# Performance work log

Measured on AMD Instinct MI355X. Metric: run time of the kernel, lower is better.

The kernel has to match this reference:

```python
import jax, jax.numpy as jnp
import numpy as np

EMBED = 1024
HEADS = 16
HEAD_DIM = EMBED // HEADS


def setup_inputs() -> dict:
    key = jax.random.key(0)
    ks = jax.random.split(key, 8)
    N, S, E = 4, 2048, EMBED
    inp = {
        "queries": jax.random.normal(ks[0], (N, S, E), dtype=jnp.float32),
        "keys": jax.random.normal(ks[1], (N, S, E), dtype=jnp.float32),
        "values": jax.random.normal(ks[2], (N, S, E), dtype=jnp.float32),
        # projection weights, stored as (in, out) so y = x @ W
        "Wq": jax.random.normal(ks[3], (E, E), dtype=jnp.float32) / np.sqrt(E),
        "Wk": jax.random.normal(ks[4], (E, E), dtype=jnp.float32) / np.sqrt(E),
        "Wv": jax.random.normal(ks[5], (E, E), dtype=jnp.float32) / np.sqrt(E),
        "Wo": jax.random.normal(ks[6], (E, E), dtype=jnp.float32) / np.sqrt(E),
        "bo": jax.random.normal(ks[7], (E,), dtype=jnp.float32) * 0.01,
    }
    return inp


def reference(queries, keys, values, Wq, Wk, Wv, Wo, bo):
    N, Sq, E = queries.shape
    Sk = keys.shape[1]
    H, D = HEADS, HEAD_DIM
    # linear projections (no bias)
    q = (queries @ Wq).reshape(N, Sq, H, D)
    k = (keys @ Wk).reshape(N, Sk, H, D)
    v = (values @ Wv).reshape(N, Sk, H, D)
    # energy: [N, H, Sq, Sk]
    energy = jnp.einsum("nqhd,nkhd->nhqk", q, k)
    attn = jax.nn.softmax(energy / np.sqrt(D).astype(np.float32), axis=3)
    # out: [N, Sq, H, D] -> [N, Sq, E]
    out = jnp.einsum("nhqk,nkhd->nqhd", attn, v).reshape(N, Sq, E)
    return out @ Wo + bo
```

## Files before the change

### kernel.cpp

```cpp
#include <hip/hip_runtime.h>
#include <hip/hip_bf16.h>

typedef __bf16 bf16;
typedef bf16 bf16x4v __attribute__((ext_vector_type(4)));
typedef bf16 bf16x8 __attribute__((ext_vector_type(8)));
typedef float f32x4 __attribute__((ext_vector_type(4)));
typedef float f32x16 __attribute__((ext_vector_type(16)));
typedef unsigned int uint;
typedef unsigned short ushort;

static constexpr int E   = 1024;
static constexpr int SEQ = 2048;
static constexpr int NB  = 4;
static constexpr int M   = NB * SEQ;

__device__ __forceinline__ void async16(const void* g, void* l) {
  __builtin_amdgcn_global_load_lds(
      (const __attribute__((address_space(1))) void*)g,
      (__attribute__((address_space(3))) void*)l, 16, 0, 0);
}

__device__ __forceinline__ uint pack2(float a, float b) {
  bf16 x = (bf16)a, y = (bf16)b;
  return (uint)__builtin_bit_cast(ushort, x) |
         ((uint)__builtin_bit_cast(ushort, y) << 16);
}

__global__ __launch_bounds__(256) void k_conv3(const float* __restrict__ s0,
                                               const float* __restrict__ s1,
                                               const float* __restrict__ s2,
                                               bf16* __restrict__ d0,
                                               bf16* __restrict__ d1,
                                               bf16* __restrict__ d2) {
  const float* src = blockIdx.z == 0 ? s0 : blockIdx.z == 1 ? s1 : s2;
  bf16* dst        = blockIdx.z == 0 ? d0 : blockIdx.z == 1 ? d1 : d2;
  size_t i = (size_t)blockIdx.x * 256 + threadIdx.x;
  const float4* s = reinterpret_cast<const float4*>(src) + i * 2;
  float4 a = s[0], b = s[1];
  bf16x8 o;
  o[0] = (bf16)a.x; o[1] = (bf16)a.y; o[2] = (bf16)a.z; o[3] = (bf16)a.w;
  o[4] = (bf16)b.x; o[5] = (bf16)b.y; o[6] = (bf16)b.z; o[7] = (bf16)b.w;
  *reinterpret_cast<bf16x8*>(dst + i * 8) = o;
}

__global__ __launch_bounds__(256) void k_convW(const float* s0, const float* s1,
                                               const float* s2, const float* s3,
                                               bf16* d0, bf16* d1, bf16* d2, bf16* d3) {
  __shared__ float tile[64][65];
  const float* W = blockIdx.z == 0 ? s0 : blockIdx.z == 1 ? s1 : blockIdx.z == 2 ? s2 : s3;
  bf16* WT       = blockIdx.z == 0 ? d0 : blockIdx.z == 1 ? d1 : blockIdx.z == 2 ? d2 : d3;
  const int tx = threadIdx.x & 63, ty = threadIdx.x >> 6;
  const int nb = blockIdx.x * 64, kb = blockIdx.y * 64;
#pragma unroll
  for (int r = 0; r < 16; ++r)
    tile[ty + r * 4][tx] = W[(size_t)(kb + ty + r * 4) * E + nb + tx];
  __syncthreads();
#pragma unroll
  for (int r = 0; r < 16; ++r)
    WT[(size_t)(nb + ty + r * 4) * E + kb + tx] = (bf16)tile[tx][ty + r * 4];
}

template <int MODE>
__global__ __launch_bounds__(256) void k_gemm(const bf16* __restrict__ A,
                                              const bf16* __restrict__ BT,
                                              void* __restrict__ Cout,
                                              const float* __restrict__ bias) {
  __shared__ __align__(16) bf16 As[2][128 * 32];
  __shared__ __align__(16) bf16 Bs[2][128 * 32];
  const int t = threadIdx.x;
  const int l = t & 63, w = t >> 6;
  const int lo = l & 15, hi = l >> 4;
  const int wm = w >> 1, wn = w & 1;
  const int m0 = blockIdx.x * 128, n0 = blockIdx.y * 128;
  f32x4 acc[4][4] = {};

  const int r0 = t >> 2, s0 = t & 3;
  const bf16* ga0 = A + (size_t)(m0 + r0) * E + s0 * 8;
  const bf16* ga1 = ga0 + (size_t)64 * E;
  const bf16* gb0 = BT + (size_t)(n0 + r0) * E + s0 * 8;
  const bf16* gb1 = gb0 + (size_t)64 * E;

  auto stage = [&](int buf, int kk) {
    char* la = (char*)As[buf] + t * 16;
    char* lb = (char*)Bs[buf] + t * 16;
    async16(ga0 + kk, la);
    async16(ga1 + kk, la + 4096);
    async16(gb0 + kk, lb);
    async16(gb1 + kk, lb + 4096);
  };

  stage(0, 0);
  __syncthreads();
  int cur = 0;
  for (int kk = 0; kk < E; kk += 32) {
    if (kk + 32 < E) stage(cur ^ 1, kk + 32);
    const bf16* AsC = As[cur];
    const bf16* BsC = Bs[cur];
    bf16x8 af[4], bfr[4];
#pragma unroll
    for (int mi = 0; mi < 4; ++mi)
      af[mi] = *(const bf16x8*)&AsC[(wm * 64 + mi * 16 + lo) * 32 + hi * 8];
#pragma unroll
    for (int ni = 0; ni < 4; ++ni)
      bfr[ni] = *(const bf16x8*)&BsC[(wn * 64 + ni * 16 + lo) * 32 + hi * 8];
    __builtin_amdgcn_s_setprio(1);
#pragma unroll
    for (int mi = 0; mi < 4; ++mi)
#pragma unroll
      for (int ni = 0; ni < 4; ++ni)
        acc[mi][ni] = __builtin_amdgcn_mfma_f32_16x16x32_bf16(af[mi], bfr[ni],
                                                              acc[mi][ni], 0, 0, 0);
    __builtin_amdgcn_s_setprio(0);
    __syncthreads();
    cur ^= 1;
  }

  const int mrow = m0 + wm * 64, ncol = n0 + wn * 64;
  if (MODE == 2) {
    float* C = (float*)Cout;
    float bv[4];
#pragma unroll
    for (int ni = 0; ni < 4; ++ni) bv[ni] = bias[ncol + ni * 16 + lo];
#pragma unroll
    for (int mi = 0; mi < 4; ++mi)
#pragma unroll
      for (int ni = 0; ni < 4; ++ni)
#pragma unroll
        for (int i = 0; i < 4; ++i)
          C[(size_t)(mrow + mi * 16 + hi * 4 + i) * E + ncol + ni * 16 + lo] =
              acc[mi][ni][i] + bv[ni];
  } else if (MODE == 1) {
    bf16* VtO = (bf16*)Cout;
#pragma unroll
    for (int mi = 0; mi < 4; ++mi) {
      int mrow_ = mrow + mi * 16 + hi * 4;
      int nb_ = mrow_ >> 11, sidx = mrow_ & 2047;
#pragma unroll
      for (int ni = 0; ni < 4; ++ni) {
        int col = ncol + ni * 16 + lo;
        bf16x4v v4;
#pragma unroll
        for (int j = 0; j < 4; ++j) v4[j] = (bf16)acc[mi][ni][j];
        *(bf16x4v*)(VtO + ((size_t)(nb_ * 16 + (col >> 6)) * 64 + (col & 63)) * SEQ + sidx) = v4;
      }
    }
  } else {
    bf16* C = (bf16*)Cout;
#pragma unroll
    for (int mi = 0; mi < 4; ++mi)
#pragma unroll
      for (int ni = 0; ni < 4; ++ni)
#pragma unroll
        for (int i = 0; i < 4; ++i)
          C[(size_t)(mrow + mi * 16 + hi * 4 + i) * E + ncol + ni * 16 + lo] =
              (bf16)acc[mi][ni][i];
  }
}

__global__ __launch_bounds__(256) void k_attn(const bf16* __restrict__ Qp,
                                              const bf16* __restrict__ Kp,
                                              const bf16* __restrict__ Vt,
                                              bf16* __restrict__ Z) {
  __shared__ __align__(16) bf16 KV[2][2][64 * 64];
  const int t = threadIdx.x, l = t & 63, w = t >> 6;
  const int qq = l & 31, hi = l >> 5, l7 = l & 7;
  const int p = blockIdx.x;
  const int lswz = (p & 7) * 128 + (p >> 3);
  const int qb = lswz & 15, nh = lswz >> 4;
  const int n = nh >> 4, h = nh & 15;
  const int q0w = qb * 128 + w * 32;

  bf16x8 qf[4];
  const bf16* qrow = Qp + (size_t)(n * SEQ + q0w + qq) * E + h * 64;
#pragma unroll
  for (int ks = 0; ks < 4; ++ks) qf[ks] = *(const bf16x8*)(qrow + ks * 16 + hi * 8);

  const bf16* kbase = Kp + (size_t)n * SEQ * E + h * 64;
  const bf16* vbase = Vt + (size_t)nh * 64 * SEQ;
  const int r_st = t >> 3, s_st = t & 7;
  const int gs = (s_st ^ (r_st & 7)) * 8;

  auto stage = [&](int buf, int kt) {
    char* lk = (char*)KV[buf][0] + t * 16;
    char* lv = (char*)KV[buf][1] + t * 16;
    async16(kbase + (size_t)(kt + r_st) * E + gs, lk);
    async16(kbase + (size_t)(kt + r_st + 32) * E + gs, lk + 4096);
    async16(vbase + (size_t)r_st * SEQ + kt + gs, lv);
    async16(vbase + (size_t)(r_st + 32) * SEQ + kt + gs, lv + 4096);
  };

  f32x16 oacc[2] = {};
  float l_r = 0.f;
  constexpr float cs = 0.18033688011112042f;

  stage(0, 0);
  __syncthreads();
  int cur = 0;
  for (int kt = 0; kt < SEQ; kt += 64) {
    if (kt + 64 < SEQ) stage(cur ^ 1, kt + 64);
    const bf16* KsC = KV[cur][0];
    const bf16* VsC = KV[cur][1];

    f32x16 sacc[2];
    __builtin_amdgcn_s_setprio(1);
#pragma unroll
    for (int kb = 0; kb < 2; ++kb) {
      f32x16 a = {};
#pragma unroll
      for (int ks = 0; ks < 4; ++ks) {
        bf16x8 kf = *(const bf16x8*)(KsC + (kb * 32 + qq) * 64 + (((ks * 2 + hi) ^ l7) * 8));
        a = __builtin_amdgcn_mfma_f32_32x32x16_bf16(kf, qf[ks], a, 0, 0, 0);
      }
      sacc[kb] = a;
    }
    __builtin_amdgcn_s_setprio(0);

    float rs = 0.f;
    uint pw[2][8];
#pragma unroll
    for (int kb = 0; kb < 2; ++kb) {
      float pv[16];
#pragma unroll
      for (int r = 0; r < 16; ++r) {
        float e = __builtin_amdgcn_exp2f(sacc[kb][r] * cs);
        pv[r] = e;
        rs += e;
      }
      uint wv[8], ex[8];
#pragma unroll
      for (int i = 0; i < 8; ++i) wv[i] = pack2(pv[2 * i], pv[2 * i + 1]);
#pragma unroll
      for (int i = 0; i < 8; ++i) ex[i] = __shfl_xor(wv[i], 32);
      pw[kb][0] = hi ? ex[2] : wv[0];
      pw[kb][1] = hi ? ex[3] : wv[1];
      pw[kb][2] = hi ? wv[2] : ex[0];
      pw[kb][3] = hi ? wv[3] : ex[1];
      pw[kb][4] = hi ? ex[6] : wv[4];
      pw[kb][5] = hi ? ex[7] : wv[5];
      pw[kb][6] = hi ? wv[6] : ex[4];
      pw[kb][7] = hi ? wv[7] : ex[5];
    }
    l_r += rs;

    __builtin_amdgcn_s_setprio(1);
#pragma unroll
    for (int d = 0; d < 2; ++d)
#pragma unroll
      for (int kb = 0; kb < 2; ++kb)
#pragma unroll
        for (int ks2 = 0; ks2 < 2; ++ks2) {
          bf16x8 pf;
          uint* pp = (uint*)&pf;
          pp[0] = pw[kb][ks2 * 4 + 0];
          pp[1] = pw[kb][ks2 * 4 + 1];
          pp[2] = pw[kb][ks2 * 4 + 2];
          pp[3] = pw[kb][ks2 * 4 + 3];
          const int ks = kb * 2 + ks2;
          bf16x8 vf = *(const bf16x8*)(VsC + (d * 32 + qq) * 64 + (((ks * 2 + hi) ^ l7) * 8));
          oacc[d] = __builtin_amdgcn_mfma_f32_32x32x16_bf16(vf, pf, oacc[d], 0, 0, 0);
        }
    __builtin_amdgcn_s_setprio(0);
    __syncthreads();
    cur ^= 1;
  }

  const float lt = l_r + __shfl_xor(l_r, 32);
  const float inv = 1.f / lt;
  bf16* zrow = Z + (size_t)(n * SEQ + q0w + qq) * E + h * 64;
#pragma unroll
  for (int d = 0; d < 2; ++d)
#pragma unroll
    for (int g = 0; g < 4; ++g) {
      bf16x4v v4;
#pragma unroll
      for (int j = 0; j < 4; ++j) v4[j] = (bf16)(oacc[d][g * 4 + j] * inv);
      *(bf16x4v*)(zrow + d * 32 + g * 8 + hi * 4) = v4;
    }
}

extern "C" void kernel_launch(void* const* d_in, const int* in_sizes, int n_in,
                              void* d_out, int out_size, void* d_ws, size_t ws_size,
                              hipStream_t stream) {
  const float* q_in = (const float*)d_in[0];
  const float* k_in = (const float*)d_in[1];
  const float* v_in = (const float*)d_in[2];
  const float* Wq   = (const float*)d_in[3];
  const float* Wk   = (const float*)d_in[4];
  const float* Wv   = (const float*)d_in[5];
  const float* Wo   = (const float*)d_in[6];
  const float* bo   = (const float*)d_in[7];

  char* ws = (char*)d_ws;
  const size_t SZ = (size_t)M * E * 2;
  bf16* qc   = (bf16*)(ws);
  bf16* kc   = (bf16*)(ws + SZ);
  bf16* vc   = (bf16*)(ws + 2 * SZ);
  bf16* qp   = (bf16*)(ws + 3 * SZ);
  bf16* kp   = (bf16*)(ws + 4 * SZ);
  bf16* vt   = (bf16*)(ws + 5 * SZ);
  bf16* zz   = (bf16*)(ws + 6 * SZ);
  bf16* wT   = (bf16*)(ws + 7 * SZ);
  bf16* wqT = wT;
  bf16* wkT = wT + (size_t)E * E;
  bf16* wvT = wT + 2 * (size_t)E * E;
  bf16* woT = wT + 3 * (size_t)E * E;

  dim3 b256(256);
  k_convW<<<dim3(16, 16, 4), b256, 0, stream>>>(Wq, Wk, Wv, Wo, wqT, wkT, wvT, woT);
  k_conv3<<<dim3(4096, 1, 3), b256, 0, stream>>>(q_in, k_in, v_in, qc, kc, vc);

  k_gemm<0><<<dim3(64, 8), b256, 0, stream>>>(qc, wqT, qp, nullptr);
  k_gemm<0><<<dim3(64, 8), b256, 0, stream>>>(kc, wkT, kp, nullptr);
  k_gemm<1><<<dim3(64, 8), b256, 0, stream>>>(vc, wvT, vt, nullptr);

  k_attn<<<dim3(1024), b256, 0, stream>>>(qp, kp, vt, zz);
  k_gemm<2><<<dim3(64, 8), b256, 0, stream>>>(zz, woT, d_out, bo);
}
```

Baseline: 242.3 us.

## Fuse fp32-to-bf16 input conversion into projection GEMMs and drop P shuffles in attention

Removes the separate activation conversion kernel. The projection GEMMs now load fp32 A tiles into registers, convert and pack them to bf16, and write them to LDS after the MFMAs, overlapping the loads with compute. The GEMM grid is remapped to a 1D swizzled block order to group blocks for L2 reuse. In attention, K rows are permuted (krow) so the exp'd P values already sit in the layout the PV MFMA expects, which eliminates the cross-half shuffle exchange. This saves a full read/write pass over the inputs but puts synchronous register-staged loads on the GEMM critical path.

```diff
diff --git a/kernel.cpp b/kernel.cpp
--- a/kernel.cpp
+++ b/kernel.cpp
@@ -24,23 +24,6 @@
   bf16 x = (bf16)a, y = (bf16)b;
   return (uint)__builtin_bit_cast(ushort, x) |
          ((uint)__builtin_bit_cast(ushort, y) << 16);
-}
-
-__global__ __launch_bounds__(256) void k_conv3(const float* __restrict__ s0,
-                                               const float* __restrict__ s1,
-                                               const float* __restrict__ s2,
-                                               bf16* __restrict__ d0,
-                                               bf16* __restrict__ d1,
-                                               bf16* __restrict__ d2) {
-  const float* src = blockIdx.z == 0 ? s0 : blockIdx.z == 1 ? s1 : s2;
-  bf16* dst        = blockIdx.z == 0 ? d0 : blockIdx.z == 1 ? d1 : d2;
-  size_t i = (size_t)blockIdx.x * 256 + threadIdx.x;
-  const float4* s = reinterpret_cast<const float4*>(src) + i * 2;
-  float4 a = s[0], b = s[1];
-  bf16x8 o;
-  o[0] = (bf16)a.x; o[1] = (bf16)a.y; o[2] = (bf16)a.z; o[3] = (bf16)a.w;
-  o[4] = (bf16)b.x; o[5] = (bf16)b.y; o[6] = (bf16)b.z; o[7] = (bf16)b.w;
-  *reinterpret_cast<bf16x8*>(dst + i * 8) = o;
 }
 
 __global__ __launch_bounds__(256) void k_convW(const float* s0, const float* s1,
@@ -61,39 +44,73 @@
 }
 
 template <int MODE>
-__global__ __launch_bounds__(256) void k_gemm(const bf16* __restrict__ A,
+__global__ __launch_bounds__(256) void k_gemm(const void* __restrict__ Ain,
                                               const bf16* __restrict__ BT,
                                               void* __restrict__ Cout,
                                               const float* __restrict__ bias) {
+  constexpr bool AF32 = (MODE != 2);
   __shared__ __align__(16) bf16 As[2][128 * 32];
   __shared__ __align__(16) bf16 Bs[2][128 * 32];
   const int t = threadIdx.x;
   const int l = t & 63, w = t >> 6;
   const int lo = l & 15, hi = l >> 4;
   const int wm = w >> 1, wn = w & 1;
-  const int m0 = blockIdx.x * 128, n0 = blockIdx.y * 128;
+  const int bid = blockIdx.x;
+  const int lb = (bid & 7) * 64 + (bid >> 3);
+  const int m0 = (lb >> 3) * 128, n0 = (lb & 7) * 128;
   f32x4 acc[4][4] = {};
 
   const int r0 = t >> 2, s0 = t & 3;
-  const bf16* ga0 = A + (size_t)(m0 + r0) * E + s0 * 8;
-  const bf16* ga1 = ga0 + (size_t)64 * E;
   const bf16* gb0 = BT + (size_t)(n0 + r0) * E + s0 * 8;
   const bf16* gb1 = gb0 + (size_t)64 * E;
-
-  auto stage = [&](int buf, int kk) {
-    char* la = (char*)As[buf] + t * 16;
-    char* lb = (char*)Bs[buf] + t * 16;
-    async16(ga0 + kk, la);
-    async16(ga1 + kk, la + 4096);
-    async16(gb0 + kk, lb);
-    async16(gb1 + kk, lb + 4096);
-  };
-
-  stage(0, 0);
+  const float* gaf = AF32 ? (const float*)Ain + (size_t)(m0 + r0) * E + s0 * 8 : nullptr;
+  const bf16*  gab = AF32 ? nullptr : (const bf16*)Ain + (size_t)(m0 + r0) * E + s0 * 8;
+
+  auto stageB = [&](int buf, int kk) {
+    char* lbp = (char*)Bs[buf] + t * 16;
+    async16(gb0 + kk, lbp);
+    async16(gb1 + kk, lbp + 4096);
+  };
+  auto loadA = [&](float4* fa, int kk) {
+    const float* p0 = gaf + kk;
+    const float* p1 = p0 + (size_t)64 * E;
+    fa[0] = *(const float4*)(p0);
+    fa[1] = *(const float4*)(p0 + 4);
+    fa[2] = *(const float4*)(p1);
+    fa[3] = *(const float4*)(p1 + 4);
+  };
+  auto writeA = [&](int buf, const float4* fa) {
+    uint4 w0, w1;
+    w0.x = pack2(fa[0].x, fa[0].y); w0.y = pack2(fa[0].z, fa[0].w);
+    w0.z = pack2(fa[1].x, fa[1].y); w0.w = pack2(fa[1].z, fa[1].w);
+    w1.x = pack2(fa[2].x, fa[2].y); w1.y = pack2(fa[2].z, fa[2].w);
+    w1.z = pack2(fa[3].x, fa[3].y); w1.w = pack2(fa[3].z, fa[3].w);
+    *(uint4*)((char*)As[buf] + t * 16) = w0;
+    *(uint4*)((char*)As[buf] + (t + 256) * 16) = w1;
+  };
+  auto stageAb = [&](int buf, int kk) {
+    char* lap = (char*)As[buf] + t * 16;
+    async16(gab + kk, lap);
+    async16(gab + (size_t)64 * E + kk, lap + 4096);
+  };
+
+  float4 fa[4];
+  if constexpr (AF32) {
+    loadA(fa, 0);
+    writeA(0, fa);
+  } else {
+    stageAb(0, 0);
+  }
+  stageB(0, 0);
   __syncthreads();
   int cur = 0;
   for (int kk = 0; kk < E; kk += 32) {
-    if (kk + 32 < E) stage(cur ^ 1, kk + 32);
+    const bool pre = (kk + 32 < E);
+    if (pre) {
+      stageB(cur ^ 1, kk + 32);
+      if constexpr (AF32) loadA(fa, kk + 32);
+      else stageAb(cur ^ 1, kk + 32);
+    }
     const bf16* AsC = As[cur];
     const bf16* BsC = Bs[cur];
     bf16x8 af[4], bfr[4];
@@ -111,6 +128,9 @@
         acc[mi][ni] = __builtin_amdgcn_mfma_f32_16x16x32_bf16(af[mi], bfr[ni],
                                                               acc[mi][ni], 0, 0, 0);
     __builtin_amdgcn_s_setprio(0);
+    if (pre) {
+      if constexpr (AF32) writeA(cur ^ 1, fa);
+    }
     __syncthreads();
     cur ^= 1;
   }
@@ -169,6 +189,7 @@
   const int qb = lswz & 15, nh = lswz >> 4;
   const int n = nh >> 4, h = nh & 15;
   const int q0w = qb * 128 + w * 32;
+  const int krow = (qq & 0x13) | ((qq & 4) << 1) | ((qq & 8) >> 1);
 
   bf16x8 qf[4];
   const bf16* qrow = Qp + (size_t)(n * SEQ + q0w + qq) * E + h * 64;
@@ -208,7 +229,7 @@
       f32x16 a = {};
 #pragma unroll
       for (int ks = 0; ks < 4; ++ks) {
-        bf16x8 kf = *(const bf16x8*)(KsC + (kb * 32 + qq) * 64 + (((ks * 2 + hi) ^ l7) * 8));
+        bf16x8 kf = *(const bf16x8*)(KsC + (kb * 32 + krow) * 64 + (((ks * 2 + hi) ^ (krow & 7)) * 8));
         a = __builtin_amdgcn_mfma_f32_32x32x16_bf16(kf, qf[ks], a, 0, 0, 0);
       }
       sacc[kb] = a;
@@ -216,7 +237,7 @@
     __builtin_amdgcn_s_setprio(0);
 
     float rs = 0.f;
-    uint pw[2][8];
+    uint wv[2][8];
 #pragma unroll
     for (int kb = 0; kb < 2; ++kb) {
       float pv[16];
@@ -226,19 +247,8 @@
         pv[r] = e;
         rs += e;
       }
-      uint wv[8], ex[8];
-#pragma unroll
-      for (int i = 0; i < 8; ++i) wv[i] = pack2(pv[2 * i], pv[2 * i + 1]);
-#pragma unroll
-      for (int i = 0; i < 8; ++i) ex[i] = __shfl_xor(wv[i], 32);
-      pw[kb][0] = hi ? ex[2] : wv[0];
-      pw[kb][1] = hi ? ex[3] : wv[1];
-      pw[kb][2] = hi ? wv[2] : ex[0];
-      pw[kb][3] = hi ? wv[3] : ex[1];
-      pw[kb][4] = hi ? ex[6] : wv[4];
-      pw[kb][5] = hi ? ex[7] : wv[5];
-      pw[kb][6] = hi ? wv[6] : ex[4];
-      pw[kb][7] = hi ? wv[7] : ex[5];
+#pragma unroll
+      for (int i = 0; i < 8; ++i) wv[kb][i] = pack2(pv[2 * i], pv[2 * i + 1]);
     }
     l_r += rs;
 
@@ -251,10 +261,10 @@
         for (int ks2 = 0; ks2 < 2; ++ks2) {
           bf16x8 pf;
           uint* pp = (uint*)&pf;
-          pp[0] = pw[kb][ks2 * 4 + 0];
-          pp[1] = pw[kb][ks2 * 4 + 1];
-          pp[2] = pw[kb][ks2 * 4 + 2];
-          pp[3] = pw[kb][ks2 * 4 + 3];
+          pp[0] = wv[kb][ks2 * 4 + 0];
+          pp[1] = wv[kb][ks2 * 4 + 1];
+          pp[2] = wv[kb][ks2 * 4 + 2];
+          pp[3] = wv[kb][ks2 * 4 + 3];
           const int ks = kb * 2 + ks2;
           bf16x8 vf = *(const bf16x8*)(VsC + (d * 32 + qq) * 64 + (((ks * 2 + hi) ^ l7) * 8));
           oacc[d] = __builtin_amdgcn_mfma_f32_32x32x16_bf16(vf, pf, oacc[d], 0, 0, 0);
@@ -292,14 +302,11 @@
 
   char* ws = (char*)d_ws;
   const size_t SZ = (size_t)M * E * 2;
-  bf16* qc   = (bf16*)(ws);
-  bf16* kc   = (bf16*)(ws + SZ);
-  bf16* vc   = (bf16*)(ws + 2 * SZ);
-  bf16* qp   = (bf16*)(ws + 3 * SZ);
-  bf16* kp   = (bf16*)(ws + 4 * SZ);
-  bf16* vt   = (bf16*)(ws + 5 * SZ);
-  bf16* zz   = (bf16*)(ws + 6 * SZ);
-  bf16* wT   = (bf16*)(ws + 7 * SZ);
+  bf16* qp = (bf16*)(ws);
+  bf16* kp = (bf16*)(ws + SZ);
+  bf16* vt = (bf16*)(ws + 2 * SZ);
+  bf16* zz = (bf16*)(ws + 3 * SZ);
+  bf16* wT = (bf16*)(ws + 4 * SZ);
   bf16* wqT = wT;
   bf16* wkT = wT + (size_t)E * E;
   bf16* wvT = wT + 2 * (size_t)E * E;
@@ -307,12 +314,11 @@
 
   dim3 b256(256);
   k_convW<<<dim3(16, 16, 4), b256, 0, stream>>>(Wq, Wk, Wv, Wo, wqT, wkT, wvT, woT);
-  k_conv3<<<dim3(4096, 1, 3), b256, 0, stream>>>(q_in, k_in, v_in, qc, kc, vc);
-
-  k_gemm<0><<<dim3(64, 8), b256, 0, stream>>>(qc, wqT, qp, nullptr);
-  k_gemm<0><<<dim3(64, 8), b256, 0, stream>>>(kc, wkT, kp, nullptr);
-  k_gemm<1><<<dim3(64, 8), b256, 0, stream>>>(vc, wvT, vt, nullptr);
+
+  k_gemm<0><<<dim3(512), b256, 0, stream>>>(q_in, wqT, qp, nullptr);
+  k_gemm<0><<<dim3(512), b256, 0, stream>>>(k_in, wkT, kp, nullptr);
+  k_gemm<1><<<dim3(512), b256, 0, stream>>>(v_in, wvT, vt, nullptr);
 
   k_attn<<<dim3(1024), b256, 0, stream>>>(qp, kp, vt, zz);
-  k_gemm<2><<<dim3(64, 8), b256, 0, stream>>>(zz, woT, d_out, bo);
-}
+  k_gemm<2><<<dim3(512), b256, 0, stream>>>(zz, woT, d_out, bo);
+}
```

After: 260.5 us. 1.07x slower.

## Process two query tiles per wave, fold softmax scale into Q projection, permute K rows

Applied to the files above, without the earlier changes.

Each wave now handles 64 query rows (two 32-row tiles) instead of 32. Each K and V fragment loaded from LDS is reused for two MFMAs, and the grid is halved. The softmax scale is folded into the Q projection GEMM epilogue (a new MODE 3), removing a multiply per exp. K rows are read in a permuted order so the P fragment layout matches the PV MFMA operand directly, which eliminates the cross-half shuffles and selects. The cost is higher register pressure (more accumulators and Q fragments) and fewer blocks to fill the device. Rounding Q to bf16 after scaling also changes numerics slightly.

```diff
diff --git a/kernel.cpp b/kernel.cpp
--- a/kernel.cpp
+++ b/kernel.cpp
@@ -145,6 +145,7 @@
       }
     }
   } else {
+    constexpr float sc = (MODE == 3) ? 0.18033688011112042f : 1.0f;
     bf16* C = (bf16*)Cout;
 #pragma unroll
     for (int mi = 0; mi < 4; ++mi)
@@ -153,27 +154,31 @@
 #pragma unroll
         for (int i = 0; i < 4; ++i)
           C[(size_t)(mrow + mi * 16 + hi * 4 + i) * E + ncol + ni * 16 + lo] =
-              (bf16)acc[mi][ni][i];
-  }
-}
-
-__global__ __launch_bounds__(256) void k_attn(const bf16* __restrict__ Qp,
-                                              const bf16* __restrict__ Kp,
-                                              const bf16* __restrict__ Vt,
-                                              bf16* __restrict__ Z) {
+              (bf16)(acc[mi][ni][i] * sc);
+  }
+}
+
+__global__ __launch_bounds__(256, 2) void k_attn(const bf16* __restrict__ Qp,
+                                                 const bf16* __restrict__ Kp,
+                                                 const bf16* __restrict__ Vt,
+                                                 bf16* __restrict__ Z) {
   __shared__ __align__(16) bf16 KV[2][2][64 * 64];
   const int t = threadIdx.x, l = t & 63, w = t >> 6;
   const int qq = l & 31, hi = l >> 5, l7 = l & 7;
   const int p = blockIdx.x;
-  const int lswz = (p & 7) * 128 + (p >> 3);
-  const int qb = lswz & 15, nh = lswz >> 4;
+  const int lswz = (p & 7) * 64 + (p >> 3);
+  const int qb = lswz & 7, nh = lswz >> 3;
   const int n = nh >> 4, h = nh & 15;
-  const int q0w = qb * 128 + w * 32;
-
-  bf16x8 qf[4];
-  const bf16* qrow = Qp + (size_t)(n * SEQ + q0w + qq) * E + h * 64;
-#pragma unroll
-  for (int ks = 0; ks < 4; ++ks) qf[ks] = *(const bf16x8*)(qrow + ks * 16 + hi * 8);
+  const int q0w = qb * 256 + w * 64;
+  const int krow = (qq & 0x13) | ((qq & 4) << 1) | ((qq & 8) >> 1);
+
+  bf16x8 qf[2][4];
+#pragma unroll
+  for (int j = 0; j < 2; ++j) {
+    const bf16* qrow = Qp + (size_t)(n * SEQ + q0w + j * 32 + qq) * E + h * 64;
+#pragma unroll
+    for (int ks = 0; ks < 4; ++ks) qf[j][ks] = *(const bf16x8*)(qrow + ks * 16 + hi * 8);
+  }
 
   const bf16* kbase = Kp + (size_t)n * SEQ * E + h * 64;
   const bf16* vbase = Vt + (size_t)nh * 64 * SEQ;
@@ -189,9 +194,8 @@
     async16(vbase + (size_t)(r_st + 32) * SEQ + kt + gs, lv + 4096);
   };
 
-  f32x16 oacc[2] = {};
-  float l_r = 0.f;
-  constexpr float cs = 0.18033688011112042f;
+  f32x16 oacc[2][2] = {};
+  float l_r[2] = {0.f, 0.f};
 
   stage(0, 0);
   __syncthreads();
@@ -201,46 +205,43 @@
     const bf16* KsC = KV[cur][0];
     const bf16* VsC = KV[cur][1];
 
-    f32x16 sacc[2];
+    f32x16 sacc[2][2];
     __builtin_amdgcn_s_setprio(1);
 #pragma unroll
     for (int kb = 0; kb < 2; ++kb) {
-      f32x16 a = {};
-#pragma unroll
-      for (int ks = 0; ks < 4; ++ks) {
-        bf16x8 kf = *(const bf16x8*)(KsC + (kb * 32 + qq) * 64 + (((ks * 2 + hi) ^ l7) * 8));
-        a = __builtin_amdgcn_mfma_f32_32x32x16_bf16(kf, qf[ks], a, 0, 0, 0);
+      bf16x8 kfr[4];
+#pragma unroll
+      for (int ks = 0; ks < 4; ++ks)
+        kfr[ks] = *(const bf16x8*)(KsC + (kb * 32 + krow) * 64 + (((ks * 2 + hi) ^ (krow & 7)) * 8));
+#pragma unroll
+      for (int j = 0; j < 2; ++j) {
+        f32x16 a = {};
+#pragma unroll
+        for (int ks = 0; ks < 4; ++ks)
+          a = __builtin_amdgcn_mfma_f32_32x32x16_bf16(kfr[ks], qf[j][ks], a, 0, 0, 0);
+        sacc[j][kb] = a;
       }
-      sacc[kb] = a;
     }
     __builtin_amdgcn_s_setprio(0);
 
-    float rs = 0.f;
-    uint pw[2][8];
-#pragma unroll
-    for (int kb = 0; kb < 2; ++kb) {
-      float pv[16];
-#pragma unroll
-      for (int r = 0; r < 16; ++r) {
-        float e = __builtin_amdgcn_exp2f(sacc[kb][r] * cs);
-        pv[r] = e;
-        rs += e;
+    uint wv[2][2][8];
+#pragma unroll
+    for (int j = 0; j < 2; ++j) {
+      float rs = 0.f;
+#pragma unroll
+      for (int kb = 0; kb < 2; ++kb) {
+        float pv[16];
+#pragma unroll
+        for (int r = 0; r < 16; ++r) {
+          float e = __builtin_amdgcn_exp2f(sacc[j][kb][r]);
+          pv[r] = e;
+          rs += e;
+        }
+#pragma unroll
+        for (int i = 0; i < 8; ++i) wv[j][kb][i] = pack2(pv[2 * i], pv[2 * i + 1]);
       }
-      uint wv[8], ex[8];
-#pragma unroll
-      for (int i = 0; i < 8; ++i) wv[i] = pack2(pv[2 * i], pv[2 * i + 1]);
-#pragma unroll
-      for (int i = 0; i < 8; ++i) ex[i] = __shfl_xor(wv[i], 32);
-      pw[kb][0] = hi ? ex[2] : wv[0];
-      pw[kb][1] = hi ? ex[3] : wv[1];
-      pw[kb][2] = hi ? wv[2] : ex[0];
-      pw[kb][3] = hi ? wv[3] : ex[1];
-      pw[kb][4] = hi ? ex[6] : wv[4];
-      pw[kb][5] = hi ? ex[7] : wv[5];
-      pw[kb][6] = hi ? wv[6] : ex[4];
-      pw[kb][7] = hi ? wv[7] : ex[5];
+      l_r[j] += rs;
     }
-    l_r += rs;
 
     __builtin_amdgcn_s_setprio(1);
 #pragma unroll
@@ -249,33 +250,39 @@
       for (int kb = 0; kb < 2; ++kb)
 #pragma unroll
         for (int ks2 = 0; ks2 < 2; ++ks2) {
-          bf16x8 pf;
-          uint* pp = (uint*)&pf;
-          pp[0] = pw[kb][ks2 * 4 + 0];
-          pp[1] = pw[kb][ks2 * 4 + 1];
-          pp[2] = pw[kb][ks2 * 4 + 2];
-          pp[3] = pw[kb][ks2 * 4 + 3];
           const int ks = kb * 2 + ks2;
           bf16x8 vf = *(const bf16x8*)(VsC + (d * 32 + qq) * 64 + (((ks * 2 + hi) ^ l7) * 8));
-          oacc[d] = __builtin_amdgcn_mfma_f32_32x32x16_bf16(vf, pf, oacc[d], 0, 0, 0);
+#pragma unroll
+          for (int j = 0; j < 2; ++j) {
+            bf16x8 pf;
+            uint* pp = (uint*)&pf;
+            pp[0] = wv[j][kb][ks2 * 4 + 0];
+            pp[1] = wv[j][kb][ks2 * 4 + 1];
+            pp[2] = wv[j][kb][ks2 * 4 + 2];
+            pp[3] = wv[j][kb][ks2 * 4 + 3];
+            oacc[j][d] = __builtin_amdgcn_mfma_f32_32x32x16_bf16(vf, pf, oacc[j][d], 0, 0, 0);
+          }
         }
     __builtin_amdgcn_s_setprio(0);
     __syncthreads();
     cur ^= 1;
   }
 
-  const float lt = l_r + __shfl_xor(l_r, 32);
-  const float inv = 1.f / lt;
-  bf16* zrow = Z + (size_t)(n * SEQ + q0w + qq) * E + h * 64;
-#pragma unroll
-  for (int d = 0; d < 2; ++d)
-#pragma unroll
-    for (int g = 0; g < 4; ++g) {
-      bf16x4v v4;
-#pragma unroll
-      for (int j = 0; j < 4; ++j) v4[j] = (bf16)(oacc[d][g * 4 + j] * inv);
-      *(bf16x4v*)(zrow + d * 32 + g * 8 + hi * 4) = v4;
-    }
+#pragma unroll
+  for (int j = 0; j < 2; ++j) {
+    const float lt = l_r[j] + __shfl_xor(l_r[j], 32);
+    const float inv = 1.f / lt;
+    bf16* zrow = Z + (size_t)(n * SEQ + q0w + j * 32 + qq) * E + h * 64;
+#pragma unroll
+    for (int d = 0; d < 2; ++d)
+#pragma unroll
+      for (int g = 0; g < 4; ++g) {
+        bf16x4v v4;
+#pragma unroll
+        for (int jj = 0; jj < 4; ++jj) v4[jj] = (bf16)(oacc[j][d][g * 4 + jj] * inv);
+        *(bf16x4v*)(zrow + d * 32 + g * 8 + hi * 4) = v4;
+      }
+  }
 }
 
 extern "C" void kernel_launch(void* const* d_in, const int* in_sizes, int n_in,
@@ -309,10 +316,10 @@
   k_convW<<<dim3(16, 16, 4), b256, 0, stream>>>(Wq, Wk, Wv, Wo, wqT, wkT, wvT, woT);
   k_conv3<<<dim3(4096, 1, 3), b256, 0, stream>>>(q_in, k_in, v_in, qc, kc, vc);
 
-  k_gemm<0><<<dim3(64, 8), b256, 0, stream>>>(qc, wqT, qp, nullptr);
+  k_gemm<3><<<dim3(64, 8), b256, 0, stream>>>(qc, wqT, qp, nullptr);
   k_gemm<0><<<dim3(64, 8), b256, 0, stream>>>(kc, wkT, kp, nullptr);
   k_gemm<1><<<dim3(64, 8), b256, 0, stream>>>(vc, wvT, vt, nullptr);
 
-  k_attn<<<dim3(1024), b256, 0, stream>>>(qp, kp, vt, zz);
+  k_attn<<<dim3(512), b256, 0, stream>>>(qp, kp, vt, zz);
   k_gemm<2><<<dim3(64, 8), b256, 0, stream>>>(zz, woT, d_out, bo);
 }
```

New measurement: 212.9 us. 1.14x faster.
